# Performance work log

Measured on AMD Instinct MI355X. Metric: run time of the kernel, lower is better.

Reference implementation:

```python
import jax, jax.numpy as jnp
import numpy as np

N_NODES = 100000
N_EDGES = 1200000
N_GRAPHS = 512
HID = 64
HEADS = 4
HEAD_DIM = 16
IN_DIM = 24
GDIM = 10
L = 2


def _ln(x, g, b, eps=1e-5):
    m = x.mean(-1, keepdims=True)
    v = x.var(-1, keepdims=True)
    return (x - m) / jnp.sqrt(v + eps) * g + b


def setup_inputs() -> dict:
    key = jax.random.key(0)
    ks = jax.random.split(key, 16)
    s = 0.1  # weight init scale to keep activations sane
    return dict(
        x=jax.random.normal(ks[0], (N_NODES, IN_DIM), jnp.float32),
        global_feats=jax.random.normal(ks[1], (N_GRAPHS, GDIM), jnp.float32),
        edge_index=jax.random.randint(ks[2], (2, N_EDGES), 0, N_NODES, dtype=jnp.int32),
        batch=jnp.sort(jax.random.randint(ks[3], (N_NODES,), 0, N_GRAPHS, dtype=jnp.int32)),
        in_w=jax.random.normal(ks[4], (IN_DIM + GDIM, HID)) * s, in_b=jnp.zeros(HID),
        in_ln_g=jnp.ones(HID), in_ln_b=jnp.zeros(HID),
        gin_eps=jnp.zeros(L),
        gin_w1=jax.random.normal(ks[5], (L, HID, 2 * HID)) * s, gin_b1=jnp.zeros((L, 2 * HID)),
        gin_bn_g=jnp.ones((L, 2 * HID)), gin_bn_b=jnp.zeros((L, 2 * HID)),
        gin_bn_m=jnp.zeros((L, 2 * HID)), gin_bn_v=jnp.ones((L, 2 * HID)),
        gin_w2=jax.random.normal(ks[6], (L, 2 * HID, HID)) * s, gin_b2=jnp.zeros((L, HID)),
        gin_ln_g=jnp.ones((L, HID)), gin_ln_b=jnp.zeros((L, HID)),
        gat_w=jax.random.normal(ks[7], (L, HID, HID)) * s,
        gat_asrc=jax.random.normal(ks[8], (L, HEADS, HEAD_DIM)) * s,
        gat_adst=jax.random.normal(ks[9], (L, HEADS, HEAD_DIM)) * s,
        gat_bias=jnp.zeros((L, HID)),
        gat_ln_g=jnp.ones((L, HID)), gat_ln_b=jnp.zeros((L, HID)),
        fus_w1=jax.random.normal(ks[10], (3 * HID, HID)) * s, fus_b1=jnp.zeros(HID),
        fus_ln_g=jnp.ones(HID), fus_ln_b=jnp.zeros(HID),
        fus_w2=jax.random.normal(ks[11], (HID, HID // 2)) * s, fus_b2=jnp.zeros(HID // 2),
        pred_w1=jax.random.normal(ks[12], (HID // 2, HID // 4)) * s, pred_b1=jnp.zeros(HID // 4),
        pred_w2=jax.random.normal(ks[13], (HID // 4, 1)) * s, pred_b2=jnp.zeros(1),
    )


def reference(x, global_feats, edge_index, batch,
              in_w, in_b, in_ln_g, in_ln_b,
              gin_eps, gin_w1, gin_b1, gin_bn_g, gin_bn_b, gin_bn_m, gin_bn_v,
              gin_w2, gin_b2, gin_ln_g, gin_ln_b,
              gat_w, gat_asrc, gat_adst, gat_bias, gat_ln_g, gat_ln_b,
              fus_w1, fus_b1, fus_ln_g, fus_ln_b, fus_w2, fus_b2,
              pred_w1, pred_b1, pred_w2, pred_b2):
    N = x.shape[0]
    src, dst = edge_index[0], edge_index[1]
    # broadcast global feats to nodes and project
    h = jnp.concatenate([x, global_feats[batch]], axis=1)  # [N, 34]
    h = jax.nn.relu(_ln(h @ in_w + in_b, in_ln_g, in_ln_b))
    # GIN stack (sum aggregation, train_eps, residual)
    for i in range(L):
        ident = h
        agg = jax.ops.segment_sum(h[src], dst, num_segments=N)
        z = (1.0 + gin_eps[i]) * h + agg
        z = z @ gin_w1[i] + gin_b1[i]
        z = (z - gin_bn_m[i]) / jnp.sqrt(gin_bn_v[i] + 1e-5) * gin_bn_g[i] + gin_bn_b[i]  # BN eval
        z = jax.nn.relu(z) @ gin_w2[i] + gin_b2[i]
        h = jax.nn.relu(_ln(z, gin_ln_g[i], gin_ln_b[i])) + ident
    gin_out = h
    # GAT stack: PyG default adds self-loops
    loop = jnp.arange(N, dtype=edge_index.dtype)
    sf = jnp.concatenate([src, loop])
    df = jnp.concatenate([dst, loop])
    for i in range(L):
        ident = h
        xp = (h @ gat_w[i]).reshape(N, HEADS, HEAD_DIM)
        asr = (xp * gat_asrc[i]).sum(-1)  # [N,H]
        adt = (xp * gat_adst[i]).sum(-1)  # [N,H]
        e = jax.nn.leaky_relu(asr[sf] + adt[df], 0.2)  # [Ef,H]
        m = jax.ops.segment_max(e, df, num_segments=N)
        p = jnp.exp(e - m[df])
        ssum = jax.ops.segment_sum(p, df, num_segments=N)
        alpha = p / ssum[df]
        out = jax.ops.segment_sum(alpha[..., None] * xp[sf], df, num_segments=N)
        out = out.reshape(N, HID) + gat_bias[i]
        h = jax.nn.elu(_ln(out, gat_ln_g[i], gat_ln_b[i])) + ident
    gat_out = h
    # triple pooling: add(gin_out) | mean(gat_out) | max(gat_out)
    add_p = jax.ops.segment_sum(gin_out, batch, num_segments=N_GRAPHS)
    cnt = jax.ops.segment_sum(jnp.ones((N, 1), gat_out.dtype), batch, num_segments=N_GRAPHS)
    mean_p = jax.ops.segment_sum(gat_out, batch, num_segments=N_GRAPHS) / jnp.maximum(cnt, 1.0)
    max_p = jax.ops.segment_max(gat_out, batch, num_segments=N_GRAPHS)
    max_p = jnp.where(jnp.isfinite(max_p), max_p, 0.0)
    pooled = jnp.concatenate([add_p, mean_p, max_p], axis=1)  # [G, 192]
    r = jax.nn.relu(_ln(pooled @ fus_w1 + fus_b1, fus_ln_g, fus_ln_b))
    r = jax.nn.relu(r @ fus_w2 + fus_b2)
    r = jax.nn.relu(r @ pred_w1 + pred_b1)
    return r @ pred_w2 + pred_b2  # [G, 1]
```

## Files before the change

kernel.cpp:

```cpp
#include <hip/hip_runtime.h>
#include <math.h>

#define N_NODES 100000
#define N_EDGES 1200000
#define N_GRAPHS 512
#define HID 64
#define HEADS 4
#define HEAD_DIM 16
#define IN_DIM 24
#define GDIM 10
#define NB_SCAN 391
#define NBLK 1563
#define ZT_S 65


__device__ __forceinline__ float wave_sum64(float v) {
#pragma unroll
  for (int m = 32; m >= 1; m >>= 1) v += __shfl_xor(v, m, 64);
  return v;
}

__device__ __forceinline__ unsigned enc_f(float f) {
  unsigned u = __float_as_uint(f);
  return (u & 0x80000000u) ? ~u : (u | 0x80000000u);
}
__device__ __forceinline__ float dec_f(unsigned u) {
  unsigned v = (u & 0x80000000u) ? (u & 0x7FFFFFFFu) : ~u;
  return __uint_as_float(v);
}

__device__ __forceinline__ float lrelu02(float x) {
  return x > 0.f ? x : 0.2f * x;
}


__global__ void k_zero_int(int* __restrict__ p, int n) {
  int i = blockIdx.x * blockDim.x + threadIdx.x;
  if (i < n) p[i] = 0;
}

__global__ void k_hist(const int* __restrict__ dst, int* __restrict__ deg) {
  int e = blockIdx.x * blockDim.x + threadIdx.x;
  if (e < N_EDGES) atomicAdd(&deg[dst[e]], 1);
}

__global__ void k_blocksum(const int* __restrict__ deg, int* __restrict__ bsum) {
  __shared__ int s[256];
  int i = blockIdx.x * 256 + threadIdx.x;
  s[threadIdx.x] = (i < N_NODES) ? deg[i] : 0;
  __syncthreads();
  for (int off = 128; off >= 1; off >>= 1) {
    if (threadIdx.x < off) s[threadIdx.x] += s[threadIdx.x + off];
    __syncthreads();
  }
  if (threadIdx.x == 0) bsum[blockIdx.x] = s[0];
}

__global__ void k_scanb(const int* __restrict__ bsum, int* __restrict__ boff) {
  __shared__ int s[512];
  int tid = threadIdx.x;
  int v = (tid < NB_SCAN) ? bsum[tid] : 0;
  s[tid] = v;
  __syncthreads();
  for (int off = 1; off < 512; off <<= 1) {
    int t = (tid >= off) ? s[tid - off] : 0;
    __syncthreads();
    s[tid] += t;
    __syncthreads();
  }
  if (tid < NB_SCAN) boff[tid] = s[tid] - v;
}

__global__ void k_offsets(const int* __restrict__ deg, const int* __restrict__ boff,
                          int* __restrict__ ptr, int* __restrict__ cur) {
  __shared__ int s[256];
  int i = blockIdx.x * 256 + threadIdx.x;
  int v = (i < N_NODES) ? deg[i] : 0;
  s[threadIdx.x] = v;
  __syncthreads();
  for (int off = 1; off < 256; off <<= 1) {
    int t = (threadIdx.x >= off) ? s[threadIdx.x - off] : 0;
    __syncthreads();
    s[threadIdx.x] += t;
    __syncthreads();
  }
  if (i < N_NODES) {
    int p = boff[blockIdx.x] + s[threadIdx.x] - v;
    ptr[i] = p;
    cur[i] = p;
  }
}

__global__ void k_scatter(const int* __restrict__ src, const int* __restrict__ dst,
                          int* __restrict__ cur, int* __restrict__ csr_src) {
  int e = blockIdx.x * blockDim.x + threadIdx.x;
  if (e < N_EDGES) {
    int pos = atomicAdd(&cur[dst[e]], 1);
    csr_src[pos] = src[e];
  }
}


__global__ void k_pool_init(float* __restrict__ add_p, float* __restrict__ sum_p,
                            unsigned* __restrict__ max_enc, float* __restrict__ cnt) {
  int i = blockIdx.x * blockDim.x + threadIdx.x;
  if (i < N_GRAPHS * HID) {
    add_p[i] = 0.f;
    sum_p[i] = 0.f;
    max_enc[i] = enc_f(-INFINITY);
  }
  if (i < N_GRAPHS) cnt[i] = 0.f;
}

__global__ void k_input(const float* __restrict__ x, const float* __restrict__ gf,
                        const int* __restrict__ batch,
                        const float* __restrict__ w, const float* __restrict__ b,
                        const float* __restrict__ lng, const float* __restrict__ lnb,
                        float* __restrict__ h) {
  int n = (blockIdx.x * blockDim.x + threadIdx.x) >> 6;
  int lane = threadIdx.x & 63;
  if (n >= N_NODES) return;
  int g = batch[n];
  float feat = 0.f;
  if (lane < IN_DIM) feat = x[n * IN_DIM + lane];
  else if (lane < IN_DIM + GDIM) feat = gf[g * GDIM + (lane - IN_DIM)];
  float acc = b[lane];
#pragma unroll
  for (int k = 0; k < IN_DIM + GDIM; ++k) {
    float fk = __shfl(feat, k, 64);
    acc += fk * w[k * HID + lane];
  }
  float mean = wave_sum64(acc) * (1.f / 64.f);
  float d = acc - mean;
  float var = wave_sum64(d * d) * (1.f / 64.f);
  float v = d * rsqrtf(var + 1e-5f) * lng[lane] + lnb[lane];
  h[n * HID + lane] = fmaxf(v, 0.f);
}

__global__ void k_gin_gather(const int* __restrict__ ptr, const int* __restrict__ deg,
                             const int* __restrict__ csr_src,
                             const float* __restrict__ h_in, float* __restrict__ z,
                             const float* __restrict__ eps_p) {
  int n = (blockIdx.x * blockDim.x + threadIdx.x) >> 6;
  int lane = threadIdx.x & 63;
  if (n >= N_NODES) return;
  int base = ptr[n], dg = deg[n];
  float hj = h_in[(size_t)n * HID + lane];
  float agg = 0.f;
  for (int c = 0; c < dg; c += 64) {
    int rem = dg - c; if (rem > 64) rem = 64;
    int idx = (lane < rem) ? csr_src[base + c + lane] : 0;
    int it = 0;
    for (; it + 8 <= rem; it += 8) {
      int s0 = __shfl(idx, it, 64);
      int s1 = __shfl(idx, it + 1, 64);
      int s2 = __shfl(idx, it + 2, 64);
      int s3 = __shfl(idx, it + 3, 64);
      int s4 = __shfl(idx, it + 4, 64);
      int s5 = __shfl(idx, it + 5, 64);
      int s6 = __shfl(idx, it + 6, 64);
      int s7 = __shfl(idx, it + 7, 64);
      float v0 = h_in[(size_t)s0 * HID + lane];
      float v1 = h_in[(size_t)s1 * HID + lane];
      float v2 = h_in[(size_t)s2 * HID + lane];
      float v3 = h_in[(size_t)s3 * HID + lane];
      float v4 = h_in[(size_t)s4 * HID + lane];
      float v5 = h_in[(size_t)s5 * HID + lane];
      float v6 = h_in[(size_t)s6 * HID + lane];
      float v7 = h_in[(size_t)s7 * HID + lane];
      agg += ((v0 + v1) + (v2 + v3)) + ((v4 + v5) + (v6 + v7));
    }
    for (; it + 4 <= rem; it += 4) {
      int s0 = __shfl(idx, it, 64);
      int s1 = __shfl(idx, it + 1, 64);
      int s2 = __shfl(idx, it + 2, 64);
      int s3 = __shfl(idx, it + 3, 64);
      float v0 = h_in[(size_t)s0 * HID + lane];
      float v1 = h_in[(size_t)s1 * HID + lane];
      float v2 = h_in[(size_t)s2 * HID + lane];
      float v3 = h_in[(size_t)s3 * HID + lane];
      agg += (v0 + v1) + (v2 + v3);
    }
    for (; it < rem; ++it) {
      int s = __shfl(idx, it, 64);
      agg += h_in[(size_t)s * HID + lane];
    }
  }
  z[(size_t)n * HID + lane] = (1.f + eps_p[0]) * hj + agg;
}

__global__ __launch_bounds__(256) void k_gin_mlp3(
    const float* __restrict__ z, const float* __restrict__ h_in,
    float* __restrict__ h_out,
    const float* __restrict__ w1, const float* __restrict__ b1,
    const float* __restrict__ bng, const float* __restrict__ bnb,
    const float* __restrict__ bnm, const float* __restrict__ bnv,
    const float* __restrict__ w2, const float* __restrict__ b2,
    const float* __restrict__ lng, const float* __restrict__ lnb,
    int do_pool, const int* __restrict__ batch,
    float* __restrict__ add_p, float* __restrict__ cnt) {
  __shared__ float smem[16384];
  float* Wbuf = smem;
  float* ZR = smem + 8192;
  int tid = threadIdx.x;
  int tx = tid & 15, ty = tid >> 4;
  int tx4 = tx * 4, ty4 = ty * 4;
  int nbase = blockIdx.x * 64;
#pragma unroll
  for (int r = 0; r < 8; ++r)
    ((float4*)Wbuf)[r * 256 + tid] = ((const float4*)w1)[r * 256 + tid];
#pragma unroll
  for (int r = 0; r < 4; ++r) {
    int e = r * 256 + tid;
    int nd = e >> 4, kq = e & 15;
    int node = nbase + nd;
    int nc = node < N_NODES ? node : N_NODES - 1;
    float4 v = ((const float4*)(z + (size_t)nc * HID))[kq];
    ZR[(kq * 4 + 0) * ZT_S + nd] = v.x;
    ZR[(kq * 4 + 1) * ZT_S + nd] = v.y;
    ZR[(kq * 4 + 2) * ZT_S + nd] = v.z;
    ZR[(kq * 4 + 3) * ZT_S + nd] = v.w;
  }
  __syncthreads();
  float c1[4][8];
#pragma unroll
  for (int mm = 0; mm < 4; ++mm)
#pragma unroll
    for (int jj = 0; jj < 8; ++jj) c1[mm][jj] = 0.f;
#pragma unroll 4
  for (int k = 0; k < 64; ++k) {
    float4 a = *(const float4*)&ZR[k * ZT_S + ty4];
    float4 b0 = *(const float4*)&Wbuf[k * 128 + tx4];
    float4 b1v = *(const float4*)&Wbuf[k * 128 + 64 + tx4];
    float av[4] = {a.x, a.y, a.z, a.w};
    float bv[8] = {b0.x, b0.y, b0.z, b0.w, b1v.x, b1v.y, b1v.z, b1v.w};
#pragma unroll
    for (int mm = 0; mm < 4; ++mm)
#pragma unroll
      for (int jj = 0; jj < 8; ++jj) c1[mm][jj] += av[mm] * bv[jj];
  }
  {
    float4 bb0 = *(const float4*)&b1[tx4];
    float4 bb1 = *(const float4*)&b1[64 + tx4];
    float4 m0 = *(const float4*)&bnm[tx4];
    float4 m1 = *(const float4*)&bnm[64 + tx4];
    float4 v0 = *(const float4*)&bnv[tx4];
    float4 v1 = *(const float4*)&bnv[64 + tx4];
    float4 g0 = *(const float4*)&bng[tx4];
    float4 g1 = *(const float4*)&bng[64 + tx4];
    float4 q0 = *(const float4*)&bnb[tx4];
    float4 q1 = *(const float4*)&bnb[64 + tx4];
    float bbv[8] = {bb0.x, bb0.y, bb0.z, bb0.w, bb1.x, bb1.y, bb1.z, bb1.w};
    float mv[8] = {m0.x, m0.y, m0.z, m0.w, m1.x, m1.y, m1.z, m1.w};
    float vv[8] = {v0.x, v0.y, v0.z, v0.w, v1.x, v1.y, v1.z, v1.w};
    float gv[8] = {g0.x, g0.y, g0.z, g0.w, g1.x, g1.y, g1.z, g1.w};
    float qv[8] = {q0.x, q0.y, q0.z, q0.w, q1.x, q1.y, q1.z, q1.w};
#pragma unroll
    for (int jj = 0; jj < 8; ++jj) {
      float sc = gv[jj] * rsqrtf(vv[jj] + 1e-5f);
      float sh = qv[jj] + (bbv[jj] - mv[jj]) * sc;
#pragma unroll
      for (int mm = 0; mm < 4; ++mm)
        c1[mm][jj] = fmaxf(c1[mm][jj] * sc + sh, 0.f);
    }
  }
  __syncthreads();
#pragma unroll
  for (int r = 0; r < 8; ++r)
    ((float4*)Wbuf)[r * 256 + tid] = ((const float4*)w2)[r * 256 + tid];
#pragma unroll
  for (int mm = 0; mm < 4; ++mm) {
    int node = ty4 + mm;
    float4 v0; v0.x = c1[mm][0]; v0.y = c1[mm][1]; v0.z = c1[mm][2]; v0.w = c1[mm][3];
    float4 v1; v1.x = c1[mm][4]; v1.y = c1[mm][5]; v1.z = c1[mm][6]; v1.w = c1[mm][7];
    *(float4*)&ZR[node * 128 + ((tx + node) & 31) * 4] = v0;
    *(float4*)&ZR[node * 128 + ((16 + tx + node) & 31) * 4] = v1;
  }
  __syncthreads();
  float c2[4][4];
#pragma unroll
  for (int mm = 0; mm < 4; ++mm)
#pragma unroll
    for (int ii = 0; ii < 4; ++ii) c2[mm][ii] = 0.f;
#pragma unroll 2
  for (int j4 = 0; j4 < 32; ++j4) {
    float4 a0 = *(const float4*)&ZR[(ty4 + 0) * 128 + ((j4 + ty4 + 0) & 31) * 4];
    float4 a1 = *(const float4*)&ZR[(ty4 + 1) * 128 + ((j4 + ty4 + 1) & 31) * 4];
    float4 a2 = *(const float4*)&ZR[(ty4 + 2) * 128 + ((j4 + ty4 + 2) & 31) * 4];
    float4 a3 = *(const float4*)&ZR[(ty4 + 3) * 128 + ((j4 + ty4 + 3) & 31) * 4];
    float4 bq0 = *(const float4*)&Wbuf[(j4 * 4 + 0) * 64 + tx4];
    float4 bq1 = *(const float4*)&Wbuf[(j4 * 4 + 1) * 64 + tx4];
    float4 bq2 = *(const float4*)&Wbuf[(j4 * 4 + 2) * 64 + tx4];
    float4 bq3 = *(const float4*)&Wbuf[(j4 * 4 + 3) * 64 + tx4];
    float4 am[4] = {a0, a1, a2, a3};
#pragma unroll
    for (int mm = 0; mm < 4; ++mm) {
      c2[mm][0] += am[mm].x * bq0.x + am[mm].y * bq1.x + am[mm].z * bq2.x + am[mm].w * bq3.x;
      c2[mm][1] += am[mm].x * bq0.y + am[mm].y * bq1.y + am[mm].z * bq2.y + am[mm].w * bq3.y;
      c2[mm][2] += am[mm].x * bq0.z + am[mm].y * bq1.z + am[mm].z * bq2.z + am[mm].w * bq3.z;
      c2[mm][3] += am[mm].x * bq0.w + am[mm].y * bq1.w + am[mm].z * bq2.w + am[mm].w * bq3.w;
    }
  }
  {
    float4 bb = *(const float4*)&b2[tx4];
    float bv[4] = {bb.x, bb.y, bb.z, bb.w};
#pragma unroll
    for (int mm = 0; mm < 4; ++mm)
#pragma unroll
      for (int ii = 0; ii < 4; ++ii) c2[mm][ii] += bv[ii];
  }
  float s1[4], s2v[4];
#pragma unroll
  for (int mm = 0; mm < 4; ++mm)
    s1[mm] = (c2[mm][0] + c2[mm][1]) + (c2[mm][2] + c2[mm][3]);
#pragma unroll
  for (int msk = 1; msk <= 8; msk <<= 1)
#pragma unroll
    for (int mm = 0; mm < 4; ++mm) s1[mm] += __shfl_xor(s1[mm], msk, 64);
  float mean[4];
#pragma unroll
  for (int mm = 0; mm < 4; ++mm) mean[mm] = s1[mm] * (1.f / 64.f);
#pragma unroll
  for (int mm = 0; mm < 4; ++mm) {
    float d0 = c2[mm][0] - mean[mm], d1 = c2[mm][1] - mean[mm];
    float d2 = c2[mm][2] - mean[mm], d3 = c2[mm][3] - mean[mm];
    s2v[mm] = (d0 * d0 + d1 * d1) + (d2 * d2 + d3 * d3);
  }
#pragma unroll
  for (int msk = 1; msk <= 8; msk <<= 1)
#pragma unroll
    for (int mm = 0; mm < 4; ++mm) s2v[mm] += __shfl_xor(s2v[mm], msk, 64);
  float4 lg = *(const float4*)&lng[tx4];
  float4 lb = *(const float4*)&lnb[tx4];
  float lgv[4] = {lg.x, lg.y, lg.z, lg.w};
  float lbv[4] = {lb.x, lb.y, lb.z, lb.w};
#pragma unroll
  for (int mm = 0; mm < 4; ++mm) {
    int node = nbase + ty4 + mm;
    if (node >= N_NODES) continue;
    float rs = rsqrtf(s2v[mm] * (1.f / 64.f) + 1e-5f);
    float4 res = *(const float4*)&h_in[(size_t)node * HID + tx4];
    float rv[4] = {res.x, res.y, res.z, res.w};
    float outv[4];
#pragma unroll
    for (int ii = 0; ii < 4; ++ii) {
      float v = (c2[mm][ii] - mean[mm]) * rs * lgv[ii] + lbv[ii];
      outv[ii] = fmaxf(v, 0.f) + rv[ii];
    }
    float4 o4; o4.x = outv[0]; o4.y = outv[1]; o4.z = outv[2]; o4.w = outv[3];
    *(float4*)&h_out[(size_t)node * HID + tx4] = o4;
    if (do_pool) {
      int g = batch[node];
#pragma unroll
      for (int ii = 0; ii < 4; ++ii)
        atomicAdd(&add_p[g * HID + tx4 + ii], outv[ii]);
      if (tx == 0) atomicAdd(&cnt[g], 1.f);
    }
  }
}

__global__ __launch_bounds__(256) void k_gat_pre3(
    const float* __restrict__ h, const float* __restrict__ w,
    const float* __restrict__ asrc, const float* __restrict__ adst,
    float* __restrict__ xp, float* __restrict__ asr, float* __restrict__ adt) {
  __shared__ float smem[64 * ZT_S + 4096];
  float* hT = smem;
  float* ws = smem + 64 * ZT_S;
  int tid = threadIdx.x;
  int tx = tid & 15, ty = tid >> 4;
  int tx4 = tx * 4, ty4 = ty * 4;
  int nbase = blockIdx.x * 64;
#pragma unroll
  for (int r = 0; r < 4; ++r) {
    int e = r * 256 + tid;
    int nd = e >> 4, kq = e & 15;
    int node = nbase + nd;
    int nc = node < N_NODES ? node : N_NODES - 1;
    float4 v = ((const float4*)(h + (size_t)nc * HID))[kq];
    hT[(kq * 4 + 0) * ZT_S + nd] = v.x;
    hT[(kq * 4 + 1) * ZT_S + nd] = v.y;
    hT[(kq * 4 + 2) * ZT_S + nd] = v.z;
    hT[(kq * 4 + 3) * ZT_S + nd] = v.w;
  }
#pragma unroll
  for (int r = 0; r < 4; ++r)
    ((float4*)ws)[r * 256 + tid] = ((const float4*)w)[r * 256 + tid];
  __syncthreads();
  float c[4][4];
#pragma unroll
  for (int mm = 0; mm < 4; ++mm)
#pragma unroll
    for (int ii = 0; ii < 4; ++ii) c[mm][ii] = 0.f;
#pragma unroll 4
  for (int k = 0; k < 64; ++k) {
    float4 a = *(const float4*)&hT[k * ZT_S + ty4];
    float4 b = *(const float4*)&ws[k * 64 + tx4];
    float av[4] = {a.x, a.y, a.z, a.w};
    float bv[4] = {b.x, b.y, b.z, b.w};
#pragma unroll
    for (int mm = 0; mm < 4; ++mm)
#pragma unroll
      for (int ii = 0; ii < 4; ++ii) c[mm][ii] += av[mm] * bv[ii];
  }
#pragma unroll
  for (int mm = 0; mm < 4; ++mm) {
    int node = nbase + ty4 + mm;
    if (node >= N_NODES) continue;
    float4 o4; o4.x = c[mm][0]; o4.y = c[mm][1]; o4.z = c[mm][2]; o4.w = c[mm][3];
    *(float4*)&xp[(size_t)node * HID + tx4] = o4;
  }
  int hd = tx >> 2, q = tx & 3;
  float4 av4 = *(const float4*)&asrc[hd * 16 + q * 4];
  float4 dv4 = *(const float4*)&adst[hd * 16 + q * 4];
  float pa[4], pd[4];
#pragma unroll
  for (int mm = 0; mm < 4; ++mm) {
    pa[mm] = c[mm][0] * av4.x + c[mm][1] * av4.y + c[mm][2] * av4.z + c[mm][3] * av4.w;
    pd[mm] = c[mm][0] * dv4.x + c[mm][1] * dv4.y + c[mm][2] * dv4.z + c[mm][3] * dv4.w;
  }
#pragma unroll
  for (int msk = 1; msk <= 2; msk <<= 1)
#pragma unroll
    for (int mm = 0; mm < 4; ++mm) {
      pa[mm] += __shfl_xor(pa[mm], msk, 64);
      pd[mm] += __shfl_xor(pd[mm], msk, 64);
    }
  if (q == 0) {
#pragma unroll
    for (int mm = 0; mm < 4; ++mm) {
      int node = nbase + ty4 + mm;
      if (node >= N_NODES) continue;
      asr[node * HEADS + hd] = pa[mm];
      adt[node * HEADS + hd] = pd[mm];
    }
  }
}

__global__ void k_gat_agg(const int* __restrict__ ptr, const int* __restrict__ deg,
                          const int* __restrict__ csr_src,
                          const float* __restrict__ xp, const float* __restrict__ asr,
                          const float* __restrict__ adt,
                          const float* __restrict__ bias,
                          const float* __restrict__ lng, const float* __restrict__ lnb,
                          float* __restrict__ h,
                          int do_pool, const int* __restrict__ batch,
                          float* __restrict__ sum_p, unsigned* __restrict__ max_enc) {
  int n = (blockIdx.x * blockDim.x + threadIdx.x) >> 6;
  int lane = threadIdx.x & 63;
  if (n >= N_NODES) return;
  int head = lane >> 4, sub = lane & 15;
  int base = ptr[n], dg = deg[n];
  float adt_d = adt[n * HEADS + head];
  float el = lrelu02(asr[n * HEADS + head] + adt_d);
  int rem0 = dg < 64 ? dg : 64;
  int idx0 = (lane < rem0) ? csr_src[base + lane] : 0;
  float pm = -1e30f, ps = 0.f;
  for (int c = 0; c < dg; c += 64) {
    int rem = dg - c; if (rem > 64) rem = 64;
    int idx = (c == 0) ? idx0 : ((lane < rem) ? csr_src[base + c + lane] : 0);
    for (int j = sub; j < rem; j += 16) {
      int s = __shfl(idx, j, 64);
      float e = lrelu02(asr[s * HEADS + head] + adt_d);
      float nm = fmaxf(pm, e);
      ps = ps * __expf(pm - nm) + __expf(e - nm);
      pm = nm;
    }
  }
#pragma unroll
  for (int msk = 1; msk <= 8; msk <<= 1) {
    float om = __shfl_xor(pm, msk, 64);
    float os = __shfl_xor(ps, msk, 64);
    float nm = fmaxf(pm, om);
    ps = ps * __expf(pm - nm) + os * __expf(om - nm);
    pm = nm;
  }
  float mfin = fmaxf(pm, el);
  float psum = ps * __expf(pm - mfin) + __expf(el - mfin);
  float o = __expf(el - mfin) * xp[(size_t)n * HID + lane];
  for (int c = 0; c < dg; c += 64) {
    int rem = dg - c; if (rem > 64) rem = 64;
    int idx = (c == 0) ? idx0 : ((lane < rem) ? csr_src[base + c + lane] : 0);
    int it = 0;
    for (; it + 4 <= rem; it += 4) {
      int s0 = __shfl(idx, it, 64);
      int s1 = __shfl(idx, it + 1, 64);
      int s2 = __shfl(idx, it + 2, 64);
      int s3 = __shfl(idx, it + 3, 64);
      float q0 = asr[s0 * HEADS + head];
      float q1 = asr[s1 * HEADS + head];
      float q2 = asr[s2 * HEADS + head];
      float q3 = asr[s3 * HEADS + head];
      float x0 = xp[(size_t)s0 * HID + lane];
      float x1 = xp[(size_t)s1 * HID + lane];
      float x2 = xp[(size_t)s2 * HID + lane];
      float x3 = xp[(size_t)s3 * HID + lane];
      float p0 = __expf(lrelu02(q0 + adt_d) - mfin);
      float p1 = __expf(lrelu02(q1 + adt_d) - mfin);
      float p2 = __expf(lrelu02(q2 + adt_d) - mfin);
      float p3 = __expf(lrelu02(q3 + adt_d) - mfin);
      o += (p0 * x0 + p1 * x1) + (p2 * x2 + p3 * x3);
    }
    for (; it < rem; ++it) {
      int s = __shfl(idx, it, 64);
      float e = lrelu02(asr[s * HEADS + head] + adt_d);
      o += __expf(e - mfin) * xp[(size_t)s * HID + lane];
    }
  }
  o = o / psum + bias[lane];
  float mean = wave_sum64(o) * (1.f / 64.f);
  float d = o - mean;
  float var = wave_sum64(d * d) * (1.f / 64.f);
  float v = d * rsqrtf(var + 1e-5f) * lng[lane] + lnb[lane];
  float e2 = v > 0.f ? v : expm1f(v);
  float hnew = e2 + h[(size_t)n * HID + lane];
  h[(size_t)n * HID + lane] = hnew;
  if (do_pool) {
    int g = batch[n];
    atomicAdd(&sum_p[g * HID + lane], hnew);
    atomicMax(&max_enc[g * HID + lane], enc_f(hnew));
  }
}

__global__ void k_final(const float* __restrict__ add_p, const float* __restrict__ sum_p,
                        const unsigned* __restrict__ max_enc, const float* __restrict__ cnt,
                        const float* __restrict__ fw1, const float* __restrict__ fb1,
                        const float* __restrict__ flng, const float* __restrict__ flnb,
                        const float* __restrict__ fw2, const float* __restrict__ fb2,
                        const float* __restrict__ pw1, const float* __restrict__ pb1,
                        const float* __restrict__ pw2, const float* __restrict__ pb2,
                        float* __restrict__ out) {
  __shared__ float buf[192];
  __shared__ float r1s[64];
  __shared__ float r2s[32];
  __shared__ float r3s[16];
  int g = blockIdx.x;
  int lane = threadIdx.x;
  float c = fmaxf(cnt[g], 1.f);
  buf[lane] = add_p[g * HID + lane];
  buf[64 + lane] = sum_p[g * HID + lane] / c;
  float mx = dec_f(max_enc[g * HID + lane]);
  if (!isfinite(mx)) mx = 0.f;
  buf[128 + lane] = mx;
  __syncthreads();
  float a = fb1[lane];
  for (int k = 0; k < 192; ++k) a += buf[k] * fw1[k * 64 + lane];
  float mean = wave_sum64(a) * (1.f / 64.f);
  float d = a - mean;
  float var = wave_sum64(d * d) * (1.f / 64.f);
  float r = fmaxf(d * rsqrtf(var + 1e-5f) * flng[lane] + flnb[lane], 0.f);
  r1s[lane] = r;
  __syncthreads();
  if (lane < 32) {
    float a2 = fb2[lane];
    for (int k = 0; k < 64; ++k) a2 += r1s[k] * fw2[k * 32 + lane];
    r2s[lane] = fmaxf(a2, 0.f);
  }
  __syncthreads();
  if (lane < 16) {
    float a3 = pb1[lane];
    for (int k = 0; k < 32; ++k) a3 += r2s[k] * pw1[k * 16 + lane];
    r3s[lane] = fmaxf(a3, 0.f);
  }
  __syncthreads();
  if (lane == 0) {
    float a4 = pb2[0];
    for (int k = 0; k < 16; ++k) a4 += r3s[k] * pw2[k];
    out[g] = a4;
  }
}


extern "C" void kernel_launch(void* const* d_in, const int* in_sizes, int n_in,
                              void* d_out, int out_size, void* d_ws, size_t ws_size,
                              hipStream_t stream) {
  const float* x = (const float*)d_in[0];
  const float* gf = (const float*)d_in[1];
  const int* ei = (const int*)d_in[2];
  const int* batch = (const int*)d_in[3];
  const float* in_w = (const float*)d_in[4];
  const float* in_b = (const float*)d_in[5];
  const float* in_ln_g = (const float*)d_in[6];
  const float* in_ln_b = (const float*)d_in[7];
  const float* gin_eps = (const float*)d_in[8];
  const float* gin_w1 = (const float*)d_in[9];
  const float* gin_b1 = (const float*)d_in[10];
  const float* gin_bn_g = (const float*)d_in[11];
  const float* gin_bn_b = (const float*)d_in[12];
  const float* gin_bn_m = (const float*)d_in[13];
  const float* gin_bn_v = (const float*)d_in[14];
  const float* gin_w2 = (const float*)d_in[15];
  const float* gin_b2 = (const float*)d_in[16];
  const float* gin_ln_g = (const float*)d_in[17];
  const float* gin_ln_b = (const float*)d_in[18];
  const float* gat_w = (const float*)d_in[19];
  const float* gat_asrc = (const float*)d_in[20];
  const float* gat_adst = (const float*)d_in[21];
  const float* gat_bias = (const float*)d_in[22];
  const float* gat_ln_g = (const float*)d_in[23];
  const float* gat_ln_b = (const float*)d_in[24];
  const float* fus_w1 = (const float*)d_in[25];
  const float* fus_b1 = (const float*)d_in[26];
  const float* fus_ln_g = (const float*)d_in[27];
  const float* fus_ln_b = (const float*)d_in[28];
  const float* fus_w2 = (const float*)d_in[29];
  const float* fus_b2 = (const float*)d_in[30];
  const float* pred_w1 = (const float*)d_in[31];
  const float* pred_b1 = (const float*)d_in[32];
  const float* pred_w2 = (const float*)d_in[33];
  const float* pred_b2 = (const float*)d_in[34];
  float* out = (float*)d_out;

  const int* src = ei;
  const int* dst = ei + N_EDGES;

  char* w = (char*)d_ws;
  float* hA = (float*)w;       w += (size_t)N_NODES * HID * 4;
  float* hB = (float*)w;       w += (size_t)N_NODES * HID * 4;
  float* zbuf = (float*)w;     w += (size_t)N_NODES * HID * 4;
  float* asr = (float*)w;      w += (size_t)N_NODES * HEADS * 4;
  float* adt = (float*)w;      w += (size_t)N_NODES * HEADS * 4;
  int* deg = (int*)w;          w += (size_t)N_NODES * 4;
  int* ptr = (int*)w;          w += (size_t)N_NODES * 4;
  int* cur = (int*)w;          w += (size_t)N_NODES * 4;
  int* csr_src = (int*)w;      w += (size_t)N_EDGES * 4;
  int* bsum = (int*)w;         w += 512 * 4;
  int* boff = (int*)w;         w += 512 * 4;
  float* add_p = (float*)w;    w += (size_t)N_GRAPHS * HID * 4;
  float* sum_p = (float*)w;    w += (size_t)N_GRAPHS * HID * 4;
  unsigned* max_enc = (unsigned*)w; w += (size_t)N_GRAPHS * HID * 4;
  float* cnt = (float*)w;      w += (size_t)N_GRAPHS * 4;

  dim3 blk(256);
  int nwb = (N_NODES + 3) / 4;
  int eb = (N_EDGES + 255) / 256;
  int nb256 = (N_NODES + 255) / 256;

  k_zero_int<<<nb256, blk, 0, stream>>>(deg, N_NODES);
  k_hist<<<eb, blk, 0, stream>>>(dst, deg);
  k_blocksum<<<NB_SCAN, blk, 0, stream>>>(deg, bsum);
  k_scanb<<<1, 512, 0, stream>>>(bsum, boff);
  k_offsets<<<NB_SCAN, blk, 0, stream>>>(deg, boff, ptr, cur);
  k_scatter<<<eb, blk, 0, stream>>>(src, dst, cur, csr_src);

  k_pool_init<<<(N_GRAPHS * HID + 255) / 256, blk, 0, stream>>>(add_p, sum_p, max_enc, cnt);
  k_input<<<nwb, blk, 0, stream>>>(x, gf, batch, in_w, in_b, in_ln_g, in_ln_b, hA);

  for (int i = 0; i < 2; ++i) {
    const float* hin = (i == 0) ? hA : hB;
    float* hout = (i == 0) ? hB : hA;
    k_gin_gather<<<nwb, blk, 0, stream>>>(ptr, deg, csr_src, hin, zbuf, gin_eps + i);
    k_gin_mlp3<<<NBLK, blk, 0, stream>>>(zbuf, hin, hout,
        gin_w1 + (size_t)i * 64 * 128, gin_b1 + i * 128,
        gin_bn_g + i * 128, gin_bn_b + i * 128, gin_bn_m + i * 128, gin_bn_v + i * 128,
        gin_w2 + (size_t)i * 128 * 64, gin_b2 + i * 64,
        gin_ln_g + i * 64, gin_ln_b + i * 64,
        (i == 1) ? 1 : 0, batch, add_p, cnt);
  }

  for (int i = 0; i < 2; ++i) {
    k_gat_pre3<<<NBLK, blk, 0, stream>>>(hA, gat_w + (size_t)i * 64 * 64,
        gat_asrc + i * HEADS * HEAD_DIM, gat_adst + i * HEADS * HEAD_DIM,
        hB, asr, adt);
    k_gat_agg<<<nwb, blk, 0, stream>>>(ptr, deg, csr_src, hB, asr, adt,
        gat_bias + i * 64, gat_ln_g + i * 64, gat_ln_b + i * 64, hA,
        (i == 1) ? 1 : 0, batch, sum_p, max_enc);
  }

  k_final<<<N_GRAPHS, 64, 0, stream>>>(add_p, sum_p, max_enc, cnt,
      fus_w1, fus_b1, fus_ln_g, fus_ln_b, fus_w2, fus_b2,
      pred_w1, pred_b1, pred_w2, pred_b2, out);
}
```

Measured before the change: 1.067 ms.

## Split GIN MLP hidden dimension into halves to shrink shared memory footprint

The fused GIN MLP kernel now computes the 128-wide hidden layer in two 64-column halves. Each half is consumed by the second GEMM through a 64x64 weight tile, so the shared buffers shrink from 64KB to about 33KB. Z is kept row-major with padding instead of transposed, and launch bounds request 4 blocks per SM. The aim is higher occupancy for this kernel, paid for with extra barriers, more weight reloads from global memory, and a second accumulator set held in registers.

```diff
diff --git a/kernel.cpp b/kernel.cpp
--- a/kernel.cpp
+++ b/kernel.cpp
@@ -12,6 +12,7 @@
 #define NB_SCAN 391
 #define NBLK 1563
 #define ZT_S 65
+#define ZA_S 68
 
 
 __device__ __forceinline__ float wave_sum64(float v) {
@@ -189,7 +190,7 @@
   z[(size_t)n * HID + lane] = (1.f + eps_p[0]) * hj + agg;
 }
 
-__global__ __launch_bounds__(256) void k_gin_mlp3(
+__global__ __launch_bounds__(256, 4) void k_gin_mlp4(
     const float* __restrict__ z, const float* __restrict__ h_in,
     float* __restrict__ h_out,
     const float* __restrict__ w1, const float* __restrict__ b1,
@@ -199,16 +200,12 @@
     const float* __restrict__ lng, const float* __restrict__ lnb,
     int do_pool, const int* __restrict__ batch,
     float* __restrict__ add_p, float* __restrict__ cnt) {
-  __shared__ float smem[16384];
-  float* Wbuf = smem;
-  float* ZR = smem + 8192;
+  __shared__ float zr[64 * ZA_S];
+  __shared__ float wbuf[64 * 64];
   int tid = threadIdx.x;
   int tx = tid & 15, ty = tid >> 4;
   int tx4 = tx * 4, ty4 = ty * 4;
   int nbase = blockIdx.x * 64;
-#pragma unroll
-  for (int r = 0; r < 8; ++r)
-    ((float4*)Wbuf)[r * 256 + tid] = ((const float4*)w1)[r * 256 + tid];
 #pragma unroll
   for (int r = 0; r < 4; ++r) {
     int e = r * 256 + tid;
@@ -216,65 +213,121 @@
     int node = nbase + nd;
     int nc = node < N_NODES ? node : N_NODES - 1;
     float4 v = ((const float4*)(z + (size_t)nc * HID))[kq];
-    ZR[(kq * 4 + 0) * ZT_S + nd] = v.x;
-    ZR[(kq * 4 + 1) * ZT_S + nd] = v.y;
-    ZR[(kq * 4 + 2) * ZT_S + nd] = v.z;
-    ZR[(kq * 4 + 3) * ZT_S + nd] = v.w;
-  }
-  __syncthreads();
-  float c1[4][8];
+    *(float4*)&zr[nd * ZA_S + kq * 4] = v;
+  }
+#pragma unroll
+  for (int r = 0; r < 4; ++r) {
+    int e = r * 256 + tid;
+    int k = e >> 4, cq = e & 15;
+    ((float4*)wbuf)[e] = *(const float4*)&w1[k * 128 + cq * 4];
+  }
+  __syncthreads();
+  float c1a[4][4];
 #pragma unroll
   for (int mm = 0; mm < 4; ++mm)
 #pragma unroll
-    for (int jj = 0; jj < 8; ++jj) c1[mm][jj] = 0.f;
+    for (int ii = 0; ii < 4; ++ii) c1a[mm][ii] = 0.f;
 #pragma unroll 4
-  for (int k = 0; k < 64; ++k) {
-    float4 a = *(const float4*)&ZR[k * ZT_S + ty4];
-    float4 b0 = *(const float4*)&Wbuf[k * 128 + tx4];
-    float4 b1v = *(const float4*)&Wbuf[k * 128 + 64 + tx4];
-    float av[4] = {a.x, a.y, a.z, a.w};
-    float bv[8] = {b0.x, b0.y, b0.z, b0.w, b1v.x, b1v.y, b1v.z, b1v.w};
-#pragma unroll
-    for (int mm = 0; mm < 4; ++mm)
-#pragma unroll
-      for (int jj = 0; jj < 8; ++jj) c1[mm][jj] += av[mm] * bv[jj];
+  for (int k4 = 0; k4 < 16; ++k4) {
+    float4 a0 = *(const float4*)&zr[(ty4 + 0) * ZA_S + k4 * 4];
+    float4 a1 = *(const float4*)&zr[(ty4 + 1) * ZA_S + k4 * 4];
+    float4 a2 = *(const float4*)&zr[(ty4 + 2) * ZA_S + k4 * 4];
+    float4 a3 = *(const float4*)&zr[(ty4 + 3) * ZA_S + k4 * 4];
+    float4 b0 = *(const float4*)&wbuf[(k4 * 4 + 0) * 64 + tx4];
+    float4 b1q = *(const float4*)&wbuf[(k4 * 4 + 1) * 64 + tx4];
+    float4 b2q = *(const float4*)&wbuf[(k4 * 4 + 2) * 64 + tx4];
+    float4 b3q = *(const float4*)&wbuf[(k4 * 4 + 3) * 64 + tx4];
+    float4 am[4] = {a0, a1, a2, a3};
+#pragma unroll
+    for (int mm = 0; mm < 4; ++mm) {
+      c1a[mm][0] += am[mm].x * b0.x + am[mm].y * b1q.x + am[mm].z * b2q.x + am[mm].w * b3q.x;
+      c1a[mm][1] += am[mm].x * b0.y + am[mm].y * b1q.y + am[mm].z * b2q.y + am[mm].w * b3q.y;
+      c1a[mm][2] += am[mm].x * b0.z + am[mm].y * b1q.z + am[mm].z * b2q.z + am[mm].w * b3q.z;
+      c1a[mm][3] += am[mm].x * b0.w + am[mm].y * b1q.w + am[mm].z * b2q.w + am[mm].w * b3q.w;
+    }
+  }
+  __syncthreads();
+#pragma unroll
+  for (int r = 0; r < 4; ++r) {
+    int e = r * 256 + tid;
+    int k = e >> 4, cq = e & 15;
+    ((float4*)wbuf)[e] = *(const float4*)&w1[k * 128 + 64 + cq * 4];
+  }
+  __syncthreads();
+  float c1b[4][4];
+#pragma unroll
+  for (int mm = 0; mm < 4; ++mm)
+#pragma unroll
+    for (int ii = 0; ii < 4; ++ii) c1b[mm][ii] = 0.f;
+#pragma unroll 4
+  for (int k4 = 0; k4 < 16; ++k4) {
+    float4 a0 = *(const float4*)&zr[(ty4 + 0) * ZA_S + k4 * 4];
+    float4 a1 = *(const float4*)&zr[(ty4 + 1) * ZA_S + k4 * 4];
+    float4 a2 = *(const float4*)&zr[(ty4 + 2) * ZA_S + k4 * 4];
+    float4 a3 = *(const float4*)&zr[(ty4 + 3) * ZA_S + k4 * 4];
+    float4 b0 = *(const float4*)&wbuf[(k4 * 4 + 0) * 64 + tx4];
+    float4 b1q = *(const float4*)&wbuf[(k4 * 4 + 1) * 64 + tx4];
+    float4 b2q = *(const float4*)&wbuf[(k4 * 4 + 2) * 64 + tx4];
+    float4 b3q = *(const float4*)&wbuf[(k4 * 4 + 3) * 64 + tx4];
+    float4 am[4] = {a0, a1, a2, a3};
+#pragma unroll
+    for (int mm = 0; mm < 4; ++mm) {
+      c1b[mm][0] += am[mm].x * b0.x + am[mm].y * b1q.x + am[mm].z * b2q.x + am[mm].w * b3q.x;
+      c1b[mm][1] += am[mm].x * b0.y + am[mm].y * b1q.y + am[mm].z * b2q.y + am[mm].w * b3q.y;
+      c1b[mm][2] += am[mm].x * b0.z + am[mm].y * b1q.z + am[mm].z * b2q.z + am[mm].w * b3q.z;
+      c1b[mm][3] += am[mm].x * b0.w + am[mm].y * b1q.w + am[mm].z * b2q.w + am[mm].w * b3q.w;
+    }
   }
   {
-    float4 bb0 = *(const float4*)&b1[tx4];
-    float4 bb1 = *(const float4*)&b1[64 + tx4];
-    float4 m0 = *(const float4*)&bnm[tx4];
-    float4 m1 = *(const float4*)&bnm[64 + tx4];
-    float4 v0 = *(const float4*)&bnv[tx4];
-    float4 v1 = *(const float4*)&bnv[64 + tx4];
-    float4 g0 = *(const float4*)&bng[tx4];
-    float4 g1 = *(const float4*)&bng[64 + tx4];
-    float4 q0 = *(const float4*)&bnb[tx4];
-    float4 q1 = *(const float4*)&bnb[64 + tx4];
-    float bbv[8] = {bb0.x, bb0.y, bb0.z, bb0.w, bb1.x, bb1.y, bb1.z, bb1.w};
-    float mv[8] = {m0.x, m0.y, m0.z, m0.w, m1.x, m1.y, m1.z, m1.w};
-    float vv[8] = {v0.x, v0.y, v0.z, v0.w, v1.x, v1.y, v1.z, v1.w};
-    float gv[8] = {g0.x, g0.y, g0.z, g0.w, g1.x, g1.y, g1.z, g1.w};
-    float qv[8] = {q0.x, q0.y, q0.z, q0.w, q1.x, q1.y, q1.z, q1.w};
-#pragma unroll
-    for (int jj = 0; jj < 8; ++jj) {
-      float sc = gv[jj] * rsqrtf(vv[jj] + 1e-5f);
-      float sh = qv[jj] + (bbv[jj] - mv[jj]) * sc;
+    float4 bb = *(const float4*)&b1[tx4];
+    float4 m = *(const float4*)&bnm[tx4];
+    float4 vv = *(const float4*)&bnv[tx4];
+    float4 g = *(const float4*)&bng[tx4];
+    float4 q = *(const float4*)&bnb[tx4];
+    float bbv[4] = {bb.x, bb.y, bb.z, bb.w};
+    float mv[4] = {m.x, m.y, m.z, m.w};
+    float vvv[4] = {vv.x, vv.y, vv.z, vv.w};
+    float gv[4] = {g.x, g.y, g.z, g.w};
+    float qv[4] = {q.x, q.y, q.z, q.w};
+#pragma unroll
+    for (int ii = 0; ii < 4; ++ii) {
+      float sc = gv[ii] * rsqrtf(vvv[ii] + 1e-5f);
+      float sh = qv[ii] + (bbv[ii] - mv[ii]) * sc;
 #pragma unroll
       for (int mm = 0; mm < 4; ++mm)
-        c1[mm][jj] = fmaxf(c1[mm][jj] * sc + sh, 0.f);
-    }
-  }
-  __syncthreads();
-#pragma unroll
-  for (int r = 0; r < 8; ++r)
-    ((float4*)Wbuf)[r * 256 + tid] = ((const float4*)w2)[r * 256 + tid];
+        c1a[mm][ii] = fmaxf(c1a[mm][ii] * sc + sh, 0.f);
+    }
+  }
+  {
+    float4 bb = *(const float4*)&b1[64 + tx4];
+    float4 m = *(const float4*)&bnm[64 + tx4];
+    float4 vv = *(const float4*)&bnv[64 + tx4];
+    float4 g = *(const float4*)&bng[64 + tx4];
+    float4 q = *(const float4*)&bnb[64 + tx4];
+    float bbv[4] = {bb.x, bb.y, bb.z, bb.w};
+    float mv[4] = {m.x, m.y, m.z, m.w};
+    float vvv[4] = {vv.x, vv.y, vv.z, vv.w};
+    float gv[4] = {g.x, g.y, g.z, g.w};
+    float qv[4] = {q.x, q.y, q.z, q.w};
+#pragma unroll
+    for (int ii = 0; ii < 4; ++ii) {
+      float sc = gv[ii] * rsqrtf(vvv[ii] + 1e-5f);
+      float sh = qv[ii] + (bbv[ii] - mv[ii]) * sc;
+#pragma unroll
+      for (int mm = 0; mm < 4; ++mm)
+        c1b[mm][ii] = fmaxf(c1b[mm][ii] * sc + sh, 0.f);
+    }
+  }
+  __syncthreads();
 #pragma unroll
   for (int mm = 0; mm < 4; ++mm) {
-    int node = ty4 + mm;
-    float4 v0; v0.x = c1[mm][0]; v0.y = c1[mm][1]; v0.z = c1[mm][2]; v0.w = c1[mm][3];
-    float4 v1; v1.x = c1[mm][4]; v1.y = c1[mm][5]; v1.z = c1[mm][6]; v1.w = c1[mm][7];
-    *(float4*)&ZR[node * 128 + ((tx + node) & 31) * 4] = v0;
-    *(float4*)&ZR[node * 128 + ((16 + tx + node) & 31) * 4] = v1;
+    float4 v; v.x = c1a[mm][0]; v.y = c1a[mm][1]; v.z = c1a[mm][2]; v.w = c1a[mm][3];
+    *(float4*)&zr[(ty4 + mm) * ZA_S + tx4] = v;
+  }
+#pragma unroll
+  for (int r = 0; r < 4; ++r) {
+    int e = r * 256 + tid;
+    ((float4*)wbuf)[e] = ((const float4*)w2)[e];
   }
   __syncthreads();
   float c2[4][4];
@@ -282,23 +335,54 @@
   for (int mm = 0; mm < 4; ++mm)
 #pragma unroll
     for (int ii = 0; ii < 4; ++ii) c2[mm][ii] = 0.f;
-#pragma unroll 2
-  for (int j4 = 0; j4 < 32; ++j4) {
-    float4 a0 = *(const float4*)&ZR[(ty4 + 0) * 128 + ((j4 + ty4 + 0) & 31) * 4];
-    float4 a1 = *(const float4*)&ZR[(ty4 + 1) * 128 + ((j4 + ty4 + 1) & 31) * 4];
-    float4 a2 = *(const float4*)&ZR[(ty4 + 2) * 128 + ((j4 + ty4 + 2) & 31) * 4];
-    float4 a3 = *(const float4*)&ZR[(ty4 + 3) * 128 + ((j4 + ty4 + 3) & 31) * 4];
-    float4 bq0 = *(const float4*)&Wbuf[(j4 * 4 + 0) * 64 + tx4];
-    float4 bq1 = *(const float4*)&Wbuf[(j4 * 4 + 1) * 64 + tx4];
-    float4 bq2 = *(const float4*)&Wbuf[(j4 * 4 + 2) * 64 + tx4];
-    float4 bq3 = *(const float4*)&Wbuf[(j4 * 4 + 3) * 64 + tx4];
+#pragma unroll 4
+  for (int j4 = 0; j4 < 16; ++j4) {
+    float4 a0 = *(const float4*)&zr[(ty4 + 0) * ZA_S + j4 * 4];
+    float4 a1 = *(const float4*)&zr[(ty4 + 1) * ZA_S + j4 * 4];
+    float4 a2 = *(const float4*)&zr[(ty4 + 2) * ZA_S + j4 * 4];
+    float4 a3 = *(const float4*)&zr[(ty4 + 3) * ZA_S + j4 * 4];
+    float4 b0 = *(const float4*)&wbuf[(j4 * 4 + 0) * 64 + tx4];
+    float4 b1q = *(const float4*)&wbuf[(j4 * 4 + 1) * 64 + tx4];
+    float4 b2q = *(const float4*)&wbuf[(j4 * 4 + 2) * 64 + tx4];
+    float4 b3q = *(const float4*)&wbuf[(j4 * 4 + 3) * 64 + tx4];
     float4 am[4] = {a0, a1, a2, a3};
 #pragma unroll
     for (int mm = 0; mm < 4; ++mm) {
-      c2[mm][0] += am[mm].x * bq0.x + am[mm].y * bq1.x + am[mm].z * bq2.x + am[mm].w * bq3.x;
-      c2[mm][1] += am[mm].x * bq0.y + am[mm].y * bq1.y + am[mm].z * bq2.y + am[mm].w * bq3.y;
-      c2[mm][2] += am[mm].x * bq0.z + am[mm].y * bq1.z + am[mm].z * bq2.z + am[mm].w * bq3.z;
-      c2[mm][3] += am[mm].x * bq0.w + am[mm].y * bq1.w + am[mm].z * bq2.w + am[mm].w * bq3.w;
+      c2[mm][0] += am[mm].x * b0.x + am[mm].y * b1q.x + am[mm].z * b2q.x + am[mm].w * b3q.x;
+      c2[mm][1] += am[mm].x * b0.y + am[mm].y * b1q.y + am[mm].z * b2q.y + am[mm].w * b3q.y;
+      c2[mm][2] += am[mm].x * b0.z + am[mm].y * b1q.z + am[mm].z * b2q.z + am[mm].w * b3q.z;
+      c2[mm][3] += am[mm].x * b0.w + am[mm].y * b1q.w + am[mm].z * b2q.w + am[mm].w * b3q.w;
+    }
+  }
+  __syncthreads();
+#pragma unroll
+  for (int mm = 0; mm < 4; ++mm) {
+    float4 v; v.x = c1b[mm][0]; v.y = c1b[mm][1]; v.z = c1b[mm][2]; v.w = c1b[mm][3];
+    *(float4*)&zr[(ty4 + mm) * ZA_S + tx4] = v;
+  }
+#pragma unroll
+  for (int r = 0; r < 4; ++r) {
+    int e = r * 256 + tid;
+    ((float4*)wbuf)[e] = ((const float4*)w2)[1024 + e];
+  }
+  __syncthreads();
+#pragma unroll 4
+  for (int j4 = 0; j4 < 16; ++j4) {
+    float4 a0 = *(const float4*)&zr[(ty4 + 0) * ZA_S + j4 * 4];
+    float4 a1 = *(const float4*)&zr[(ty4 + 1) * ZA_S + j4 * 4];
+    float4 a2 = *(const float4*)&zr[(ty4 + 2) * ZA_S + j4 * 4];
+    float4 a3 = *(const float4*)&zr[(ty4 + 3) * ZA_S + j4 * 4];
+    float4 b0 = *(const float4*)&wbuf[(j4 * 4 + 0) * 64 + tx4];
+    float4 b1q = *(const float4*)&wbuf[(j4 * 4 + 1) * 64 + tx4];
+    float4 b2q = *(const float4*)&wbuf[(j4 * 4 + 2) * 64 + tx4];
+    float4 b3q = *(const float4*)&wbuf[(j4 * 4 + 3) * 64 + tx4];
+    float4 am[4] = {a0, a1, a2, a3};
+#pragma unroll
+    for (int mm = 0; mm < 4; ++mm) {
+      c2[mm][0] += am[mm].x * b0.x + am[mm].y * b1q.x + am[mm].z * b2q.x + am[mm].w * b3q.x;
+      c2[mm][1] += am[mm].x * b0.y + am[mm].y * b1q.y + am[mm].z * b2q.y + am[mm].w * b3q.y;
+      c2[mm][2] += am[mm].x * b0.z + am[mm].y * b1q.z + am[mm].z * b2q.z + am[mm].w * b3q.z;
+      c2[mm][3] += am[mm].x * b0.w + am[mm].y * b1q.w + am[mm].z * b2q.w + am[mm].w * b3q.w;
     }
   }
   {
@@ -649,7 +733,7 @@
     const float* hin = (i == 0) ? hA : hB;
     float* hout = (i == 0) ? hB : hA;
     k_gin_gather<<<nwb, blk, 0, stream>>>(ptr, deg, csr_src, hin, zbuf, gin_eps + i);
-    k_gin_mlp3<<<NBLK, blk, 0, stream>>>(zbuf, hin, hout,
+    k_gin_mlp4<<<NBLK, blk, 0, stream>>>(zbuf, hin, hout,
         gin_w1 + (size_t)i * 64 * 128, gin_b1 + i * 128,
         gin_bn_g + i * 128, gin_bn_b + i * 128, gin_bn_m + i * 128, gin_bn_v + i * 128,
         gin_w2 + (size_t)i * 128 * 64, gin_b2 + i * 64,
```

After: 995.3 us. -6.7%, faster.
